# Kernel optimization log

Measured on AMD Instinct MI355X. Metric: run time of the kernel, lower is better.

Reference implementation:

```python
import jax, jax.numpy as jnp
import numpy as np

HIDDEN = 256
KSQ = 9  # 3x3 kernel


def _unfold3(x):
    # torch F.unfold(x, 3, padding=1): (N, C*9, H, W), channel-major then (ky,kx)
    N, C, H, W = x.shape
    xp = jnp.pad(x, ((0, 0), (0, 0), (1, 1), (1, 1)))
    patches = [xp[:, :, i:i + H, j:j + W] for i in range(3) for j in range(3)]
    cols = jnp.stack(patches, axis=2)  # (N, C, 9, H, W)
    return cols.reshape(N, C * KSQ, H, W)


def setup_inputs() -> dict:
    key = jax.random.key(0)
    ks = jax.random.split(key, 8)
    N, C, H, W = 1, 3, 512, 512
    OH, OW = 1024, 1024
    pos_mat = jax.random.uniform(ks[0], (N, OH, OW, 3), dtype=jnp.float32)
    mapping_mat = jax.random.randint(ks[1], (OH, OW, 2), 0, 512, dtype=jnp.int64)
    feats = jax.random.normal(ks[2], (N, C, H, W), dtype=jnp.float32)
    depth = jax.random.normal(ks[3], (N, 1, H, W), dtype=jnp.float32)
    out_ch = 1
    K = KSQ * 3 * out_ch  # 27
    W1 = jax.random.normal(ks[4], (HIDDEN, 3), dtype=jnp.float32) * 0.05
    b1 = jnp.zeros((HIDDEN,), dtype=jnp.float32)
    W2 = jax.random.normal(ks[5], (K, HIDDEN), dtype=jnp.float32) * 0.05
    b2 = jnp.zeros((K,), dtype=jnp.float32)
    return {"pos_mat": pos_mat, "mapping_mat": mapping_mat, "feats": feats,
            "depth": depth, "W1": W1, "b1": b1, "W2": W2, "b2": b2}


def reference(pos_mat, mapping_mat, feats, depth, W1, b1, W2, b2):
    N, C, H, W = feats.shape
    _, OH, OW, _ = pos_mat.shape
    P = OH * OW
    # meta-MLP: per-pixel kernel weights (P, 27)
    h = jax.nn.leaky_relu(pos_mat.reshape(P, 3) @ W1.T + b1, negative_slope=0.01)
    local_weight = h @ W2.T + b2  # (P, K)
    # im2col + irregular gather via mapping_mat
    cols = _unfold3(feats)  # (N, C*9, H, W)
    feat = cols[:, :, mapping_mat[:, :, 0], mapping_mat[:, :, 1]]  # (N, C*9, OH, OW)
    feat = feat.reshape(N, C * KSQ, P).transpose(0, 2, 1)  # (N, P, K)
    # batched tiny matmul: per-pixel dot product
    out = jnp.einsum('npk,pk->np', feat, local_weight)
    return out.reshape(N, 1, OH, OW)
```

## Files before the change

### kernel.cpp

```cpp
#include <hip/hip_runtime.h>

#define HID 256
#define K27 27

typedef __attribute__((ext_vector_type(8))) short    bf16x8;
typedef __attribute__((ext_vector_type(4))) float    f32x4;
typedef __attribute__((ext_vector_type(4))) unsigned u32x4;

static __device__ __forceinline__ unsigned short f2bf(float f) {
    union { float f; unsigned u; } v; v.f = f;
    return (unsigned short)((v.u + 0x7FFFu + ((v.u >> 16) & 1u)) >> 16);
}
static __device__ __forceinline__ unsigned pack2bf(float lo, float hi) {
    unsigned r;
    asm("v_cvt_pk_bf16_f32 %0, %1, %2" : "=v"(r) : "v"(lo), "v"(hi));
    return r;
}
static __device__ __forceinline__ bf16x8 as_bf16x8(u32x4 u) {
    return __builtin_bit_cast(bf16x8, u);
}
static __device__ __forceinline__ bf16x8 frag1(unsigned u) {
    u32x4 t = {u, 0u, 0u, 0u};
    return __builtin_bit_cast(bf16x8, t);
}
static __device__ __forceinline__ float lk(float x) {
    return fmaxf(x, 0.01f * x);
}

__global__ __launch_bounds__(256, 4) void mapnet_v6(
    const float* __restrict__ pos,
    const int*   __restrict__ mapping,
    const float* __restrict__ feats,
    const float* __restrict__ W1,
    const float* __restrict__ b1,
    const float* __restrict__ W2,
    const float* __restrict__ b2,
    float* __restrict__ out)
{
    __shared__ unsigned sW1f[16][64];
    __shared__ bf16x8   sB[16][64];

    const int tid = threadIdx.x;

    for (int e = tid; e < 1024; e += 256) {
        const int jt = e >> 6, l = e & 63;
        const int gg = l >> 4, cc = l & 15;
        const int j = jt * 16 + cc;
        const float val = (gg < 3) ? W1[3 * j + gg] : b1[j];
        sW1f[jt][l] = pack2bf(val, 0.0f);
    }
    for (int e = tid; e < 1024; e += 256) {
        const int kcnt = e >> 6, l = e & 63;
        const int kc = kcnt >> 1, nt = kcnt & 1;
        const int gg = l >> 4, cc = l & 15;
        const int n = nt * 16 + cc;
        const int jbase = kc * 32 + 4 * gg;
        u32x4 bb;
        #pragma unroll
        for (int i = 0; i < 4; ++i) {
            const int jlo = jbase + 16 * (i >> 1) + 2 * (i & 1);
            float f0 = 0.f, f1 = 0.f;
            if (n < K27) { f0 = W2[n * HID + jlo]; f1 = W2[n * HID + jlo + 1]; }
            bb[i] = (unsigned)f2bf(f0) | ((unsigned)f2bf(f1) << 16);
        }
        sB[kcnt][l] = as_bf16x8(bb);
    }
    __syncthreads();

    const int lane = tid & 63, wid = tid >> 6;
    const int g = lane >> 4, col = lane & 15;

    const float b2A = b2[col];
    const float b2B = (col < K27 - 16) ? b2[16 + col] : 0.0f;
    const int kA = col;
    const int cA = kA/9, dyA = (kA%9)/3 - 1, dxA = (kA%9)%3 - 1;
    const int kB = min(16 + col, K27 - 1);
    const int cB = kB/9, dyB = (kB%9)/3 - 1, dxB = (kB%9)%3 - 1;

    const float* fbaseA = feats + cA * (512*512);
    const float* fbaseB = feats + cB * (512*512);
    const int2*  map2   = (const int2*)mapping;

    const int w = blockIdx.x * 4 + wid;

    for (int it = 0; it < 4; ++it) {
        const int tb0 = (w * 8 + it * 2) * 16;
        const int tb1 = tb0 + 16;

        const float q00 = pos[3*(tb0+col)], q01 = pos[3*(tb0+col)+1], q02 = pos[3*(tb0+col)+2];
        const float q10 = pos[3*(tb1+col)], q11 = pos[3*(tb1+col)+1], q12 = pos[3*(tb1+col)+2];
        const float v0 = (g == 0) ? q00 : (g == 1) ? q01 : (g == 2) ? q02 : 1.0f;
        const float v1 = (g == 0) ? q10 : (g == 1) ? q11 : (g == 2) ? q12 : 1.0f;
        const bf16x8 pB0 = frag1(pack2bf(v0, 0.0f));
        const bf16x8 pB1 = frag1(pack2bf(v1, 0.0f));

        float fvA[2][4], fvB[2][4];
        #pragma unroll
        for (int tt = 0; tt < 2; ++tt) {
            const int tb = tt ? tb1 : tb0;
            #pragma unroll
            for (int r = 0; r < 4; ++r) {
                const int2 mp = map2[tb + g*4 + r];
                const int my = mp.x, mx = mp.y;
                int y  = my + dyA, x  = mx + dxA;
                int yc = min(max(y,0),511), xc = min(max(x,0),511);
                float f = fbaseA[yc*512 + xc];
                fvA[tt][r] = (((unsigned)y | (unsigned)x) < 512u) ? f : 0.f;
                int y2 = my + dyB, x2 = mx + dxB;
                int yc2 = min(max(y2,0),511), xc2 = min(max(x2,0),511);
                float f2 = fbaseB[yc2*512 + xc2];
                fvB[tt][r] = (((unsigned)y2 | (unsigned)x2) < 512u) ? f2 : 0.f;
            }
        }

        f32x4 acc00 = {b2A,b2A,b2A,b2A}, acc01 = {b2B,b2B,b2B,b2B};
        f32x4 acc10 = {b2A,b2A,b2A,b2A}, acc11 = {b2B,b2B,b2B,b2B};
        const f32x4 zero = {0.f, 0.f, 0.f, 0.f};

        #pragma unroll
        for (int kc = 0; kc < 8; ++kc) {
            const bf16x8 wA0 = frag1(sW1f[2*kc    ][lane]);
            const bf16x8 wA1 = frag1(sW1f[2*kc + 1][lane]);

            const f32x4 c00 = __builtin_amdgcn_mfma_f32_16x16x32_bf16(wA0, pB0, zero, 0,0,0);
            const f32x4 c01 = __builtin_amdgcn_mfma_f32_16x16x32_bf16(wA1, pB0, zero, 0,0,0);
            const f32x4 c10 = __builtin_amdgcn_mfma_f32_16x16x32_bf16(wA0, pB1, zero, 0,0,0);
            const f32x4 c11 = __builtin_amdgcn_mfma_f32_16x16x32_bf16(wA1, pB1, zero, 0,0,0);

            u32x4 a0, a1;
            a0[0] = pack2bf(lk(c00[0]), lk(c00[1]));
            a0[1] = pack2bf(lk(c00[2]), lk(c00[3]));
            a0[2] = pack2bf(lk(c01[0]), lk(c01[1]));
            a0[3] = pack2bf(lk(c01[2]), lk(c01[3]));
            a1[0] = pack2bf(lk(c10[0]), lk(c10[1]));
            a1[1] = pack2bf(lk(c10[2]), lk(c10[3]));
            a1[2] = pack2bf(lk(c11[0]), lk(c11[1]));
            a1[3] = pack2bf(lk(c11[2]), lk(c11[3]));
            const bf16x8 av0 = as_bf16x8(a0);
            const bf16x8 av1 = as_bf16x8(a1);

            const bf16x8 bv0 = sB[kc*2    ][lane];
            const bf16x8 bv1 = sB[kc*2 + 1][lane];
            acc00 = __builtin_amdgcn_mfma_f32_16x16x32_bf16(av0, bv0, acc00, 0,0,0);
            acc01 = __builtin_amdgcn_mfma_f32_16x16x32_bf16(av0, bv1, acc01, 0,0,0);
            acc10 = __builtin_amdgcn_mfma_f32_16x16x32_bf16(av1, bv0, acc10, 0,0,0);
            acc11 = __builtin_amdgcn_mfma_f32_16x16x32_bf16(av1, bv1, acc11, 0,0,0);
        }

        #pragma unroll
        for (int tt = 0; tt < 2; ++tt) {
            const int tb = tt ? tb1 : tb0;
            const f32x4 aA = tt ? acc10 : acc00;
            const f32x4 aB = tt ? acc11 : acc01;
            #pragma unroll
            for (int r = 0; r < 4; ++r) {
                float s = aA[r] * fvA[tt][r] + aB[r] * fvB[tt][r];
                s += __shfl_xor(s, 1);
                s += __shfl_xor(s, 2);
                s += __shfl_xor(s, 4);
                s += __shfl_xor(s, 8);
                if (col == r) out[tb + g*4 + r] = s;
            }
        }
    }
}

extern "C" void kernel_launch(void* const* d_in, const int* in_sizes, int n_in,
                              void* d_out, int out_size, void* d_ws, size_t ws_size,
                              hipStream_t stream) {
    const float* pos     = (const float*)d_in[0];
    const int*   mapping = (const int*)d_in[1];
    const float* feats   = (const float*)d_in[2];
    const float* W1      = (const float*)d_in[4];
    const float* b1      = (const float*)d_in[5];
    const float* W2      = (const float*)d_in[6];
    const float* b2      = (const float*)d_in[7];
    float* out = (float*)d_out;

    mapnet_v6<<<2048, 256, 0, stream>>>(pos, mapping, feats, W1, b1, W2, b2, out);
}
```

Before: 80.39 us.

## Prefetch next mapping/pos in registers, keep W1 in VGPRs, DPP reductions

Loads of the mapping indices and positions for the next iteration are issued before the current iteration's MFMA work, so their latency overlaps with compute. The bf16-packed W1 fragments now live in per-thread registers instead of LDS, which removes one shared-memory staging loop and its LDS reads. The 16-lane shuffle-xor reduction is replaced by DPP quad_perm and row_ror adds. In exchange, register pressure rises, which could limit occupancy under the 256x4 launch bounds.

```diff
diff --git a/kernel.cpp b/kernel.cpp
--- a/kernel.cpp
+++ b/kernel.cpp
@@ -26,8 +26,11 @@
 static __device__ __forceinline__ float lk(float x) {
     return fmaxf(x, 0.01f * x);
 }
-
-__global__ __launch_bounds__(256, 4) void mapnet_v6(
+#define DPP_ADD(s, ctrl) \
+    s += __builtin_bit_cast(float, __builtin_amdgcn_update_dpp( \
+            0, __builtin_bit_cast(int, s), ctrl, 0xF, 0xF, true))
+
+__global__ __launch_bounds__(256, 4) void mapnet_v7(
     const float* __restrict__ pos,
     const int*   __restrict__ mapping,
     const float* __restrict__ feats,
@@ -37,18 +40,9 @@
     const float* __restrict__ b2,
     float* __restrict__ out)
 {
-    __shared__ unsigned sW1f[16][64];
-    __shared__ bf16x8   sB[16][64];
+    __shared__ bf16x8 sB[16][64];
 
     const int tid = threadIdx.x;
-
-    for (int e = tid; e < 1024; e += 256) {
-        const int jt = e >> 6, l = e & 63;
-        const int gg = l >> 4, cc = l & 15;
-        const int j = jt * 16 + cc;
-        const float val = (gg < 3) ? W1[3 * j + gg] : b1[j];
-        sW1f[jt][l] = pack2bf(val, 0.0f);
-    }
     for (int e = tid; e < 1024; e += 256) {
         const int kcnt = e >> 6, l = e & 63;
         const int kc = kcnt >> 1, nt = kcnt & 1;
@@ -70,6 +64,14 @@
     const int lane = tid & 63, wid = tid >> 6;
     const int g = lane >> 4, col = lane & 15;
 
+    unsigned w1r[16];
+    #pragma unroll
+    for (int jt = 0; jt < 16; ++jt) {
+        const int j = jt * 16 + col;
+        const float val = (g < 3) ? W1[3 * j + g] : b1[j];
+        w1r[jt] = pack2bf(val, 0.0f);
+    }
+
     const float b2A = b2[col];
     const float b2B = (col < K27 - 16) ? b2[16 + col] : 0.0f;
     const int kA = col;
@@ -83,25 +85,33 @@
 
     const int w = blockIdx.x * 4 + wid;
 
+    int2  mpc[8];
+    float pc[6];
+    {
+        const int tb0 = (w * 8) * 16, tb1 = tb0 + 16;
+        #pragma unroll
+        for (int tt = 0; tt < 2; ++tt)
+            #pragma unroll
+            for (int r = 0; r < 4; ++r)
+                mpc[tt*4 + r] = map2[(tt ? tb1 : tb0) + g*4 + r];
+        pc[0] = pos[3*(tb0+col)]; pc[1] = pos[3*(tb0+col)+1]; pc[2] = pos[3*(tb0+col)+2];
+        pc[3] = pos[3*(tb1+col)]; pc[4] = pos[3*(tb1+col)+1]; pc[5] = pos[3*(tb1+col)+2];
+    }
+
     for (int it = 0; it < 4; ++it) {
-        const int tb0 = (w * 8 + it * 2) * 16;
-        const int tb1 = tb0 + 16;
-
-        const float q00 = pos[3*(tb0+col)], q01 = pos[3*(tb0+col)+1], q02 = pos[3*(tb0+col)+2];
-        const float q10 = pos[3*(tb1+col)], q11 = pos[3*(tb1+col)+1], q12 = pos[3*(tb1+col)+2];
-        const float v0 = (g == 0) ? q00 : (g == 1) ? q01 : (g == 2) ? q02 : 1.0f;
-        const float v1 = (g == 0) ? q10 : (g == 1) ? q11 : (g == 2) ? q12 : 1.0f;
+        const int tb0 = (w * 8 + it * 2) * 16, tb1 = tb0 + 16;
+
+        const float v0 = (g == 0) ? pc[0] : (g == 1) ? pc[1] : (g == 2) ? pc[2] : 1.0f;
+        const float v1 = (g == 0) ? pc[3] : (g == 1) ? pc[4] : (g == 2) ? pc[5] : 1.0f;
         const bf16x8 pB0 = frag1(pack2bf(v0, 0.0f));
         const bf16x8 pB1 = frag1(pack2bf(v1, 0.0f));
 
         float fvA[2][4], fvB[2][4];
         #pragma unroll
         for (int tt = 0; tt < 2; ++tt) {
-            const int tb = tt ? tb1 : tb0;
             #pragma unroll
             for (int r = 0; r < 4; ++r) {
-                const int2 mp = map2[tb + g*4 + r];
-                const int my = mp.x, mx = mp.y;
+                const int my = mpc[tt*4 + r].x, mx = mpc[tt*4 + r].y;
                 int y  = my + dyA, x  = mx + dxA;
                 int yc = min(max(y,0),511), xc = min(max(x,0),511);
                 float f = fbaseA[yc*512 + xc];
@@ -113,14 +123,32 @@
             }
         }
 
+        int2  mpn[8];
+        float pn[6];
+        if (it < 3) {
+            const int nb0 = (w * 8 + (it+1) * 2) * 16, nb1 = nb0 + 16;
+            #pragma unroll
+            for (int tt = 0; tt < 2; ++tt)
+                #pragma unroll
+                for (int r = 0; r < 4; ++r)
+                    mpn[tt*4 + r] = map2[(tt ? nb1 : nb0) + g*4 + r];
+            pn[0] = pos[3*(nb0+col)]; pn[1] = pos[3*(nb0+col)+1]; pn[2] = pos[3*(nb0+col)+2];
+            pn[3] = pos[3*(nb1+col)]; pn[4] = pos[3*(nb1+col)+1]; pn[5] = pos[3*(nb1+col)+2];
+        } else {
+            #pragma unroll
+            for (int i = 0; i < 8; ++i) mpn[i] = mpc[i];
+            #pragma unroll
+            for (int i = 0; i < 6; ++i) pn[i] = pc[i];
+        }
+
         f32x4 acc00 = {b2A,b2A,b2A,b2A}, acc01 = {b2B,b2B,b2B,b2B};
         f32x4 acc10 = {b2A,b2A,b2A,b2A}, acc11 = {b2B,b2B,b2B,b2B};
         const f32x4 zero = {0.f, 0.f, 0.f, 0.f};
 
         #pragma unroll
         for (int kc = 0; kc < 8; ++kc) {
-            const bf16x8 wA0 = frag1(sW1f[2*kc    ][lane]);
-            const bf16x8 wA1 = frag1(sW1f[2*kc + 1][lane]);
+            const bf16x8 wA0 = frag1(w1r[2*kc    ]);
+            const bf16x8 wA1 = frag1(w1r[2*kc + 1]);
 
             const f32x4 c00 = __builtin_amdgcn_mfma_f32_16x16x32_bf16(wA0, pB0, zero, 0,0,0);
             const f32x4 c01 = __builtin_amdgcn_mfma_f32_16x16x32_bf16(wA1, pB0, zero, 0,0,0);
@@ -155,13 +183,18 @@
             #pragma unroll
             for (int r = 0; r < 4; ++r) {
                 float s = aA[r] * fvA[tt][r] + aB[r] * fvB[tt][r];
-                s += __shfl_xor(s, 1);
-                s += __shfl_xor(s, 2);
-                s += __shfl_xor(s, 4);
-                s += __shfl_xor(s, 8);
+                DPP_ADD(s, 0xB1);
+                DPP_ADD(s, 0x4E);
+                DPP_ADD(s, 0x124);
+                DPP_ADD(s, 0x128);
                 if (col == r) out[tb + g*4 + r] = s;
             }
         }
+
+        #pragma unroll
+        for (int i = 0; i < 8; ++i) mpc[i] = mpn[i];
+        #pragma unroll
+        for (int i = 0; i < 6; ++i) pc[i] = pn[i];
     }
 }
 
@@ -177,5 +210,5 @@
     const float* b2      = (const float*)d_in[7];
     float* out = (float*)d_out;
 
-    mapnet_v6<<<2048, 256, 0, stream>>>(pos, mapping, feats, W1, b1, W2, b2, out);
-}
+    mapnet_v7<<<2048, 256, 0, stream>>>(pos, mapping, feats, W1, b1, W2, b2, out);
+}
```

New measurement: 193.4 us. 141% more time.
